# Optimization experiments

Hardware: AMD Instinct MI355X
Metric: run time of the kernel (lower is better)

Reference implementation:

```python
import jax, jax.numpy as jnp
import numpy as np

D_MODEL = 1024
NUM_HEADS = 16
HEAD = D_MODEL // NUM_HEADS
SCALE = float(np.sqrt(D_MODEL))  # note: sqrt(d_model), as in source
LN_EPS = 1e-5


def setup_inputs() -> dict:
    key = jax.random.key(0)
    ks = jax.random.split(key, 12)
    B, Sq, Skv = 2, 2048, 2048
    s = 0.02
    return {
        "x": jax.random.normal(ks[0], (B, Sq, D_MODEL), jnp.float32),
        "enc_output": jax.random.normal(ks[1], (B, Skv, D_MODEL), jnp.float32),
        "Wq": jax.random.normal(ks[2], (D_MODEL, D_MODEL), jnp.float32) * s,
        "bq": jnp.zeros((D_MODEL,), jnp.float32),
        "Wk": jax.random.normal(ks[3], (D_MODEL, D_MODEL), jnp.float32) * s,
        "bk": jnp.zeros((D_MODEL,), jnp.float32),
        "Wv": jax.random.normal(ks[4], (D_MODEL, D_MODEL), jnp.float32) * s,
        "bv": jnp.zeros((D_MODEL,), jnp.float32),
        "Wo": jax.random.normal(ks[5], (D_MODEL, D_MODEL), jnp.float32) * s,
        "bo": jnp.zeros((D_MODEL,), jnp.float32),
        "gamma": jnp.ones((D_MODEL,), jnp.float32),
        "beta": jnp.zeros((D_MODEL,), jnp.float32),
    }


def _split_heads(t):
    B, S, _ = t.shape
    return t.reshape(B, S, NUM_HEADS, HEAD).transpose(0, 2, 1, 3)  # [B,H,S,hd]


def reference(x, enc_output, Wq, bq, Wk, bk, Wv, bv, Wo, bo, gamma, beta):
    q = _split_heads(x @ Wq.T + bq)           # [B,H,Sq,hd]
    k = _split_heads(enc_output @ Wk.T + bk)  # [B,H,Skv,hd]
    v = _split_heads(enc_output @ Wv.T + bv)  # [B,H,Skv,hd]
    scores = jnp.einsum("bhqd,bhkd->bhqk", q, k) / SCALE
    attn_weights = jax.nn.softmax(scores, axis=-1)  # dropout p=0 -> identity
    ctx = jnp.einsum("bhqk,bhkd->bhqd", attn_weights, v)
    B, H, Sq, hd = ctx.shape
    ctx = ctx.transpose(0, 2, 1, 3).reshape(B, Sq, H * hd)
    proj = ctx @ Wo.T + bo
    y = x + proj
    mu = jnp.mean(y, axis=-1, keepdims=True)
    var = jnp.var(y, axis=-1, keepdims=True)
    out = (y - mu) * jax.lax.rsqrt(var + LN_EPS) * gamma + beta
    return out, attn_weights
```

## Files before the change

kernel.cpp:

```cpp
#include <hip/hip_runtime.h>

typedef __attribute__((ext_vector_type(4))) float f32x4;
typedef __attribute__((ext_vector_type(8))) short bf16x8;
typedef __attribute__((ext_vector_type(4))) short s16x4;
typedef __attribute__((ext_vector_type(4))) unsigned u32x4;
typedef unsigned short u16;

#define GLOAD_LDS16(g, l)                                                      \
  __builtin_amdgcn_global_load_lds(                                            \
      (__attribute__((address_space(1))) const void*)(g),                      \
      (__attribute__((address_space(3))) void*)(l), 16, 0, 0)

static __device__ __forceinline__ u16 f2b(float f) {
  unsigned u = __builtin_bit_cast(unsigned, f);
  unsigned r = (u + 0x7fffu + ((u >> 16) & 1u)) >> 16;
  return (u16)r;
}

static __device__ __forceinline__ unsigned pk2(float lo, float hi) {
  unsigned r;
  asm("v_cvt_pk_bf16_f32 %0, %1, %2" : "=v"(r) : "v"(lo), "v"(hi));
  return r;
}

static __device__ __forceinline__ f32x4 mfma16(bf16x8 a, bf16x8 b, f32x4 c) {
  return __builtin_amdgcn_mfma_f32_16x16x32_bf16(a, b, c, 0, 0, 0);
}

static __device__ __forceinline__ int fsw(int row) {
  return (row & 7) ^ ((row & 8) >> 1);
}

__global__ __launch_bounds__(256) void cvt_bf16(const float* __restrict__ in,
                                                u16* __restrict__ out, int n4) {
  int i = blockIdx.x * 256 + threadIdx.x;
  int stride = gridDim.x * 256;
  for (; i < n4; i += stride) {
    float4 v = ((const float4*)in)[i];
    s16x4 o;
    o[0] = (short)f2b(v.x);
    o[1] = (short)f2b(v.y);
    o[2] = (short)f2b(v.z);
    o[3] = (short)f2b(v.w);
    ((s16x4*)out)[i] = o;
  }
}

__global__ __launch_bounds__(256) void cvt_w4(const float* __restrict__ w0,
                                              const float* __restrict__ w1,
                                              const float* __restrict__ w2,
                                              const float* __restrict__ w3,
                                              u16* __restrict__ o0,
                                              u16* __restrict__ o1,
                                              u16* __restrict__ o2,
                                              u16* __restrict__ o3) {
  int y = blockIdx.y;
  const float* in = (y == 0) ? w0 : (y == 1) ? w1 : (y == 2) ? w2 : w3;
  u16* out = (y == 0) ? o0 : (y == 1) ? o1 : (y == 2) ? o2 : o3;
  const int n4 = 262144;
  int i = blockIdx.x * 256 + threadIdx.x;
  int stride = gridDim.x * 256;
  for (; i < n4; i += stride) {
    float4 v = ((const float4*)in)[i];
    s16x4 o;
    o[0] = (short)f2b(v.x);
    o[1] = (short)f2b(v.y);
    o[2] = (short)f2b(v.z);
    o[3] = (short)f2b(v.w);
    ((s16x4*)out)[i] = o;
  }
}

#define QSCALE 0.0450842200278f
__global__ __launch_bounds__(256) void gemm_qkv3(
    const u16* __restrict__ xb, const u16* __restrict__ eb,
    const u16* __restrict__ Wqb, const u16* __restrict__ Wkb,
    const u16* __restrict__ Wvb, const float* __restrict__ bq,
    const float* __restrict__ bk, const float* __restrict__ bv,
    u16* __restrict__ Qd, u16* __restrict__ Kd, u16* __restrict__ Vtd) {
  __shared__ __align__(16) u16 As[128 * 32];
  __shared__ __align__(16) u16 Bs[128 * 32];
  const int K = 1024;
  int z = blockIdx.z;
  const u16* A = (z == 0) ? xb : eb;
  const u16* W = (z == 0) ? Wqb : (z == 1) ? Wkb : Wvb;
  const float* bias = (z == 0) ? bq : (z == 1) ? bk : bv;

  int tid = threadIdx.x;
  int w = tid >> 6, lane = tid & 63;
  int wr = w >> 1, wc = w & 1;
  int r16 = lane & 15, c4 = lane >> 4;
  int m0 = blockIdx.y * 128, n0 = blockIdx.x * 128;
  int srow = tid >> 2;
  int scol = (tid & 3) * 8;

  f32x4 acc[4][4] = {};

  const u16* ga0 = A + (size_t)(m0 + srow) * K + scol;
  const u16* gb0 = W + (size_t)(n0 + srow) * K + scol;
  char* asb = (char*)As + w * 1024;
  char* bsb = (char*)Bs + w * 1024;

  for (int k0 = 0; k0 < K; k0 += 32) {
    GLOAD_LDS16(ga0 + k0, asb);
    GLOAD_LDS16(ga0 + 64 * K + k0, asb + 4096);
    GLOAD_LDS16(gb0 + k0, bsb);
    GLOAD_LDS16(gb0 + 64 * K + k0, bsb + 4096);
    __syncthreads();
    bf16x8 af[4], bfr[4];
#pragma unroll
    for (int i = 0; i < 4; ++i)
      af[i] = *(const bf16x8*)(As + (wr * 64 + i * 16 + r16) * 32 + c4 * 8);
#pragma unroll
    for (int j = 0; j < 4; ++j)
      bfr[j] = *(const bf16x8*)(Bs + (wc * 64 + j * 16 + r16) * 32 + c4 * 8);
#pragma unroll
    for (int i = 0; i < 4; ++i)
#pragma unroll
      for (int j = 0; j < 4; ++j) acc[i][j] = mfma16(af[i], bfr[j], acc[i][j]);
    __syncthreads();
  }

  if (z < 2) {
    float oscale = (z == 0) ? QSCALE : 1.0f;
    u16* dst = (z == 0) ? Qd : Kd;
#pragma unroll
    for (int i = 0; i < 4; ++i) {
      int m = m0 + wr * 64 + i * 16 + c4 * 4;
      int b = m >> 11, s = m & 2047;
#pragma unroll
      for (int j = 0; j < 4; ++j) {
        int n = n0 + wc * 64 + j * 16 + r16;
        int h = n >> 6, d = n & 63;
        float bv = bias[n];
        u16* dp = dst + (((size_t)(b * 16 + h) * 2048 + s) * 64 + d);
#pragma unroll
        for (int r = 0; r < 4; ++r)
          dp[(size_t)r * 64] = f2b((acc[i][j][r] + bv) * oscale);
      }
    }
  } else {
#pragma unroll
    for (int i = 0; i < 4; ++i) {
      int m = m0 + wr * 64 + i * 16 + c4 * 4;
      int b = m >> 11, s = m & 2047;
#pragma unroll
      for (int j = 0; j < 4; ++j) {
        int n = n0 + wc * 64 + j * 16 + r16;
        int h = n >> 6, d = n & 63;
        float bv = bias[n];
        s16x4 o4;
#pragma unroll
        for (int r = 0; r < 4; ++r) o4[r] = (short)f2b(acc[i][j][r] + bv);
        *(s16x4*)(Vtd + ((size_t)((b * 16 + h) * 64 + d)) * 2048 + s) = o4;
      }
    }
  }
}

__global__ __launch_bounds__(256) void gemm_out(const u16* __restrict__ A,
                                                const u16* __restrict__ W,
                                                const float* __restrict__ bias,
                                                const float* __restrict__ X,
                                                float* __restrict__ Y) {
  __shared__ __align__(16) u16 As[128 * 32];
  __shared__ __align__(16) u16 Bs[128 * 32];
  const int K = 1024;
  int tid = threadIdx.x;
  int w = tid >> 6, lane = tid & 63;
  int wr = w >> 1, wc = w & 1;
  int r16 = lane & 15, c4 = lane >> 4;
  int m0 = blockIdx.y * 128, n0 = blockIdx.x * 128;
  int srow = tid >> 2;
  int scol = (tid & 3) * 8;

  f32x4 acc[4][4] = {};

  const u16* ga0 = A + (size_t)(m0 + srow) * K + scol;
  const u16* gb0 = W + (size_t)(n0 + srow) * K + scol;
  char* asb = (char*)As + w * 1024;
  char* bsb = (char*)Bs + w * 1024;

  for (int k0 = 0; k0 < K; k0 += 32) {
    GLOAD_LDS16(ga0 + k0, asb);
    GLOAD_LDS16(ga0 + 64 * K + k0, asb + 4096);
    GLOAD_LDS16(gb0 + k0, bsb);
    GLOAD_LDS16(gb0 + 64 * K + k0, bsb + 4096);
    __syncthreads();
    bf16x8 af[4], bfr[4];
#pragma unroll
    for (int i = 0; i < 4; ++i)
      af[i] = *(const bf16x8*)(As + (wr * 64 + i * 16 + r16) * 32 + c4 * 8);
#pragma unroll
    for (int j = 0; j < 4; ++j)
      bfr[j] = *(const bf16x8*)(Bs + (wc * 64 + j * 16 + r16) * 32 + c4 * 8);
#pragma unroll
    for (int i = 0; i < 4; ++i)
#pragma unroll
      for (int j = 0; j < 4; ++j) acc[i][j] = mfma16(af[i], bfr[j], acc[i][j]);
    __syncthreads();
  }

#pragma unroll
  for (int i = 0; i < 4; ++i) {
    int m = m0 + wr * 64 + i * 16 + c4 * 4;
#pragma unroll
    for (int j = 0; j < 4; ++j) {
      int n = n0 + wc * 64 + j * 16 + r16;
      float bv = bias[n];
#pragma unroll
      for (int r = 0; r < 4; ++r) {
        size_t idx = (size_t)(m + r) * 1024 + n;
        Y[idx] = acc[i][j][r] + bv + X[idx];
      }
    }
  }
}

__global__ __launch_bounds__(256, 2) void attn_k(const u16* __restrict__ Q,
                                                 const u16* __restrict__ Kg,
                                                 const u16* __restrict__ Vt,
                                                 float* __restrict__ attnw,
                                                 u16* __restrict__ ctx) {
  __shared__ __align__(16) u16 Klds[2][64 * 64];
  __shared__ __align__(16) u16 Vlds[2][64 * 64];

  int tid = threadIdx.x;
  int w = tid >> 6, lane = tid & 63;
  int r16 = lane & 15, c4 = lane >> 4;
  int id = blockIdx.x;
  int bh = id & 31, qt = id >> 5;
  int b = bh >> 4, h = bh & 15;
  int q0 = qt * 128 + w * 32;

  const u16* Qp = Q + ((size_t)bh * 2048 + q0) * 64;
  const u16* Kp = Kg + (size_t)bh * 2048 * 64;
  const u16* Vp = Vt + (size_t)bh * 64 * 2048;

  bf16x8 qf[2][2];
#pragma unroll
  for (int hh = 0; hh < 2; ++hh)
#pragma unroll
    for (int ch = 0; ch < 2; ++ch)
      qf[hh][ch] = *(const bf16x8*)(Qp + (size_t)(hh * 16 + r16) * 64 +
                                    ch * 32 + c4 * 8);

  int perm0 = ((r16 >> 2) << 3) + (r16 & 3);
  int srow0 = w * 8 + (lane >> 3);
  int sc = lane & 7;

#define STAGE_K(bufi, kv)                                                      \
  {                                                                            \
    _Pragma("unroll") for (int i = 0; i < 2; ++i) {                            \
      int row = i * 32 + srow0;                                                \
      int ch = sc ^ fsw(row);                                                  \
      GLOAD_LDS16(Kp + (size_t)((kv) + row) * 64 + ch * 8,                     \
                  (u16*)&Klds[bufi][0] + w * 512 + i * 2048);                  \
    }                                                                          \
  }
#define STAGE_V(bufi, kv)                                                      \
  {                                                                            \
    _Pragma("unroll") for (int i = 0; i < 2; ++i) {                            \
      int row = i * 32 + srow0;                                                \
      int ch = sc ^ fsw(row);                                                  \
      GLOAD_LDS16(Vp + (size_t)row * 2048 + (kv) + ch * 8,                     \
                  (u16*)&Vlds[bufi][0] + w * 512 + i * 2048);                  \
    }                                                                          \
  }
#define LDSF(base, row, chunk)                                                 \
  (*(const bf16x8*)((base) + (row) * 64 + (((chunk) ^ fsw(row)) << 3)))
#define WAIT_BAR(n)                                                            \
  {                                                                            \
    asm volatile("s_waitcnt vmcnt(" #n ")" ::: "memory");                      \
    __builtin_amdgcn_s_barrier();                                              \
  }

  float sumA = 0.f, sumB = 0.f;
  STAGE_K(0, 0);
  WAIT_BAR(0);
  int buf = 0;
  for (int kv0 = 0; kv0 < 2048; kv0 += 64) {
    if (kv0 + 64 < 2048) STAGE_K(buf ^ 1, kv0 + 64);
    const u16* Kb = &Klds[buf][0];
#pragma unroll
    for (int s = 0; s < 2; ++s) {
      int ra = s * 32 + perm0;
      bf16x8 k00 = LDSF(Kb, ra, c4);
      bf16x8 k01 = LDSF(Kb, ra, c4 + 4);
      bf16x8 k10 = LDSF(Kb, ra + 4, c4);
      bf16x8 k11 = LDSF(Kb, ra + 4, c4 + 4);
      f32x4 s0A = {}, s1A = {}, s0B = {}, s1B = {};
      __builtin_amdgcn_s_setprio(1);
      s0A = mfma16(k00, qf[0][0], s0A);
      s0A = mfma16(k01, qf[0][1], s0A);
      s1A = mfma16(k10, qf[0][0], s1A);
      s1A = mfma16(k11, qf[0][1], s1A);
      s0B = mfma16(k00, qf[1][0], s0B);
      s0B = mfma16(k01, qf[1][1], s0B);
      s1B = mfma16(k10, qf[1][0], s1B);
      s1B = mfma16(k11, qf[1][1], s1B);
      __builtin_amdgcn_s_setprio(0);
#pragma unroll
      for (int r = 0; r < 4; ++r) {
        sumA += __builtin_amdgcn_exp2f(s0A[r]) + __builtin_amdgcn_exp2f(s1A[r]);
        sumB += __builtin_amdgcn_exp2f(s0B[r]) + __builtin_amdgcn_exp2f(s1B[r]);
      }
    }
    WAIT_BAR(0);
    buf ^= 1;
  }
  sumA += __shfl_xor(sumA, 16, 64);
  sumA += __shfl_xor(sumA, 32, 64);
  sumB += __shfl_xor(sumB, 16, 64);
  sumB += __shfl_xor(sumB, 32, 64);
  float nlsA = -__log2f(sumA);
  float nlsB = -__log2f(sumB);

  f32x4 oA[4] = {}, oB[4] = {};
  float* apA = attnw + ((size_t)bh * 2048 + q0 + r16) * 2048;
  float* apB = apA + (size_t)16 * 2048;
  STAGE_K(0, 0);
  STAGE_V(0, 0);
  WAIT_BAR(0);
  buf = 0;
  for (int kv0 = 0; kv0 < 2048; kv0 += 64) {
    if (kv0 + 64 < 2048) {
      STAGE_K(buf ^ 1, kv0 + 64);
      STAGE_V(buf ^ 1, kv0 + 64);
    }
    const u16* Kb = &Klds[buf][0];
    const u16* Vb = &Vlds[buf][0];
#pragma unroll
    for (int s = 0; s < 2; ++s) {
      int ra = s * 32 + perm0;
      bf16x8 k00 = LDSF(Kb, ra, c4);
      bf16x8 k01 = LDSF(Kb, ra, c4 + 4);
      bf16x8 k10 = LDSF(Kb, ra + 4, c4);
      bf16x8 k11 = LDSF(Kb, ra + 4, c4 + 4);
      f32x4 s0A = {}, s1A = {}, s0B = {}, s1B = {};
      __builtin_amdgcn_s_setprio(1);
      s0A = mfma16(k00, qf[0][0], s0A);
      s0A = mfma16(k01, qf[0][1], s0A);
      s1A = mfma16(k10, qf[0][0], s1A);
      s1A = mfma16(k11, qf[0][1], s1A);
      s0B = mfma16(k00, qf[1][0], s0B);
      s0B = mfma16(k01, qf[1][1], s0B);
      s1B = mfma16(k10, qf[1][0], s1B);
      s1B = mfma16(k11, qf[1][1], s1B);
      __builtin_amdgcn_s_setprio(0);
      f32x4 p0A, p1A, p0B, p1B;
#pragma unroll
      for (int r = 0; r < 4; ++r) {
        p0A[r] = __builtin_amdgcn_exp2f(s0A[r] + nlsA);
        p1A[r] = __builtin_amdgcn_exp2f(s1A[r] + nlsA);
        p0B[r] = __builtin_amdgcn_exp2f(s0B[r] + nlsB);
        p1B[r] = __builtin_amdgcn_exp2f(s1B[r] + nlsB);
      }
      u32x4 pkA, pkB;
      pkA[0] = pk2(p0A[0], p0A[1]);
      pkA[1] = pk2(p0A[2], p0A[3]);
      pkA[2] = pk2(p1A[0], p1A[1]);
      pkA[3] = pk2(p1A[2], p1A[3]);
      pkB[0] = pk2(p0B[0], p0B[1]);
      pkB[1] = pk2(p0B[2], p0B[3]);
      pkB[2] = pk2(p1B[0], p1B[1]);
      pkB[3] = pk2(p1B[2], p1B[3]);
      bf16x8 pfA = __builtin_bit_cast(bf16x8, pkA);
      bf16x8 pfB = __builtin_bit_cast(bf16x8, pkB);
      bf16x8 v0 = LDSF(Vb, 0 * 16 + r16, s * 4 + c4);
      bf16x8 v1 = LDSF(Vb, 1 * 16 + r16, s * 4 + c4);
      bf16x8 v2 = LDSF(Vb, 2 * 16 + r16, s * 4 + c4);
      bf16x8 v3 = LDSF(Vb, 3 * 16 + r16, s * 4 + c4);
      __builtin_amdgcn_s_setprio(1);
      oA[0] = mfma16(pfA, v0, oA[0]);
      oA[1] = mfma16(pfA, v1, oA[1]);
      oA[2] = mfma16(pfA, v2, oA[2]);
      oA[3] = mfma16(pfA, v3, oA[3]);
      oB[0] = mfma16(pfB, v0, oB[0]);
      oB[1] = mfma16(pfB, v1, oB[1]);
      oB[2] = mfma16(pfB, v2, oB[2]);
      oB[3] = mfma16(pfB, v3, oB[3]);
      __builtin_amdgcn_s_setprio(0);
      int kvc = kv0 + s * 32 + c4 * 8;
      *(f32x4*)(apA + kvc) = p0A;
      *(f32x4*)(apA + kvc + 4) = p1A;
      *(f32x4*)(apB + kvc) = p0B;
      *(f32x4*)(apB + kvc + 4) = p1B;
    }
    WAIT_BAR(8);
    buf ^= 1;
  }

#pragma unroll
  for (int dt = 0; dt < 4; ++dt)
#pragma unroll
    for (int r = 0; r < 4; ++r) {
      ctx[((size_t)(b * 2048 + q0 + c4 * 4 + r)) * 1024 + h * 64 + dt * 16 +
          r16] = f2b(oA[dt][r]);
      ctx[((size_t)(b * 2048 + q0 + 16 + c4 * 4 + r)) * 1024 + h * 64 +
          dt * 16 + r16] = f2b(oB[dt][r]);
    }
#undef STAGE_K
#undef STAGE_V
#undef LDSF
#undef WAIT_BAR
}

__global__ __launch_bounds__(256) void ln_k(const float* __restrict__ Y,
                                            const float* __restrict__ gamma,
                                            const float* __restrict__ beta,
                                            float* __restrict__ out) {
  int row = blockIdx.x * 4 + (threadIdx.x >> 6);
  int lane = threadIdx.x & 63;
  const float* yr = Y + (size_t)row * 1024;
  float4 v[4];
  float sum = 0.f, sq = 0.f;
#pragma unroll
  for (int i = 0; i < 4; ++i) {
    v[i] = *(const float4*)(yr + i * 256 + lane * 4);
    sum += v[i].x + v[i].y + v[i].z + v[i].w;
    sq += v[i].x * v[i].x + v[i].y * v[i].y + v[i].z * v[i].z + v[i].w * v[i].w;
  }
#pragma unroll
  for (int m = 1; m < 64; m <<= 1) {
    sum += __shfl_xor(sum, m, 64);
    sq += __shfl_xor(sq, m, 64);
  }
  float mu = sum * (1.f / 1024.f);
  float var = sq * (1.f / 1024.f) - mu * mu;
  float rs = rsqrtf(var + 1e-5f);
  float* orow = out + (size_t)row * 1024;
#pragma unroll
  for (int i = 0; i < 4; ++i) {
    int c = i * 256 + lane * 4;
    float4 g = *(const float4*)(gamma + c);
    float4 be = *(const float4*)(beta + c);
    float4 o;
    o.x = (v[i].x - mu) * rs * g.x + be.x;
    o.y = (v[i].y - mu) * rs * g.y + be.y;
    o.z = (v[i].z - mu) * rs * g.z + be.z;
    o.w = (v[i].w - mu) * rs * g.w + be.w;
    *(float4*)(orow + c) = o;
  }
}

extern "C" void kernel_launch(void* const* d_in, const int* in_sizes, int n_in,
                              void* d_out, int out_size, void* d_ws,
                              size_t ws_size, hipStream_t stream) {
  const float* x = (const float*)d_in[0];
  const float* enc = (const float*)d_in[1];
  const float* Wq = (const float*)d_in[2];
  const float* bq = (const float*)d_in[3];
  const float* Wk = (const float*)d_in[4];
  const float* bk = (const float*)d_in[5];
  const float* Wv = (const float*)d_in[6];
  const float* bv = (const float*)d_in[7];
  const float* Wo = (const float*)d_in[8];
  const float* bo = (const float*)d_in[9];
  const float* gamma = (const float*)d_in[10];
  const float* beta = (const float*)d_in[11];

  float* out = (float*)d_out;
  float* attnw = out + (size_t)4194304;

  char* ws = (char*)d_ws;
  u16* xb = (u16*)(ws + (size_t)0);
  u16* eb = (u16*)(ws + ((size_t)8 << 20));
  u16* Wqb = (u16*)(ws + ((size_t)16 << 20));
  u16* Wkb = (u16*)(ws + ((size_t)18 << 20));
  u16* Wvb = (u16*)(ws + ((size_t)20 << 20));
  u16* Wob = (u16*)(ws + ((size_t)22 << 20));
  u16* Qws = (u16*)(ws + ((size_t)24 << 20));
  u16* Kws = (u16*)(ws + ((size_t)32 << 20));
  u16* Vt = (u16*)(ws + ((size_t)48 << 20));
  u16* ctx = (u16*)(ws + ((size_t)40 << 20));
  float* Yws = (float*)(ws + (size_t)0);

  cvt_bf16<<<dim3(1024), 256, 0, stream>>>(x, xb, 1048576);
  cvt_bf16<<<dim3(1024), 256, 0, stream>>>(enc, eb, 1048576);
  cvt_w4<<<dim3(256, 4), 256, 0, stream>>>(Wq, Wk, Wv, Wo, Wqb, Wkb, Wvb, Wob);

  gemm_qkv3<<<dim3(8, 32, 3), 256, 0, stream>>>(xb, eb, Wqb, Wkb, Wvb, bq, bk,
                                                bv, Qws, Kws, Vt);

  attn_k<<<dim3(512), 256, 0, stream>>>(Qws, Kws, Vt, attnw, ctx);

  gemm_out<<<dim3(8, 32), 256, 0, stream>>>(ctx, Wob, bo, x, Yws);

  ln_k<<<dim3(1024), 256, 0, stream>>>(Yws, gamma, beta, out);
}
```

Measured before the change: 304.5 us.

## Load V fragments directly from global into registers, bypassing LDS staging

The second attention pass no longer stages V tiles through shared memory. Each wave instead loads its V fragments straight from global memory into registers, double-buffered one 32-column half-step ahead, and the vmcnt wait is raised to account for the extra in-flight loads. This removes LDS traffic and the V share of the barrier-synchronised staging, and halves the attention kernel's LDS footprint. In exchange every wave fetches V redundantly from global/L2 (four waves per block), register pressure rises, and the vmcnt accounting becomes more fragile.

```diff
diff --git a/kernel.cpp b/kernel.cpp
--- a/kernel.cpp
+++ b/kernel.cpp
@@ -223,7 +223,6 @@
                                                  float* __restrict__ attnw,
                                                  u16* __restrict__ ctx) {
   __shared__ __align__(16) u16 Klds[2][64 * 64];
-  __shared__ __align__(16) u16 Vlds[2][64 * 64];
 
   int tid = threadIdx.x;
   int w = tid >> 6, lane = tid & 63;
@@ -248,6 +247,7 @@
   int perm0 = ((r16 >> 2) << 3) + (r16 & 3);
   int srow0 = w * 8 + (lane >> 3);
   int sc = lane & 7;
+  const u16* vbase = Vp + (size_t)r16 * 2048 + c4 * 8;
 
 #define STAGE_K(bufi, kv)                                                      \
   {                                                                            \
@@ -258,21 +258,17 @@
                   (u16*)&Klds[bufi][0] + w * 512 + i * 2048);                  \
     }                                                                          \
   }
-#define STAGE_V(bufi, kv)                                                      \
-  {                                                                            \
-    _Pragma("unroll") for (int i = 0; i < 2; ++i) {                            \
-      int row = i * 32 + srow0;                                                \
-      int ch = sc ^ fsw(row);                                                  \
-      GLOAD_LDS16(Vp + (size_t)row * 2048 + (kv) + ch * 8,                     \
-                  (u16*)&Vlds[bufi][0] + w * 512 + i * 2048);                  \
-    }                                                                          \
-  }
 #define LDSF(base, row, chunk)                                                 \
   (*(const bf16x8*)((base) + (row) * 64 + (((chunk) ^ fsw(row)) << 3)))
 #define WAIT_BAR(n)                                                            \
   {                                                                            \
     asm volatile("s_waitcnt vmcnt(" #n ")" ::: "memory");                      \
     __builtin_amdgcn_s_barrier();                                              \
+  }
+#define VLOAD(dst, kvc)                                                        \
+  {                                                                            \
+    _Pragma("unroll") for (int dt = 0; dt < 4; ++dt) (dst)[dt] =               \
+        *(const bf16x8*)(vbase + (size_t)(dt * 16) * 2048 + (kvc));            \
   }
 
   float sumA = 0.f, sumB = 0.f;
@@ -319,17 +315,14 @@
   f32x4 oA[4] = {}, oB[4] = {};
   float* apA = attnw + ((size_t)bh * 2048 + q0 + r16) * 2048;
   float* apB = apA + (size_t)16 * 2048;
+  bf16x8 vg[4], vh[4];
+  VLOAD(vg, 0);
   STAGE_K(0, 0);
-  STAGE_V(0, 0);
   WAIT_BAR(0);
   buf = 0;
   for (int kv0 = 0; kv0 < 2048; kv0 += 64) {
-    if (kv0 + 64 < 2048) {
-      STAGE_K(buf ^ 1, kv0 + 64);
-      STAGE_V(buf ^ 1, kv0 + 64);
-    }
+    if (kv0 + 64 < 2048) STAGE_K(buf ^ 1, kv0 + 64);
     const u16* Kb = &Klds[buf][0];
-    const u16* Vb = &Vlds[buf][0];
 #pragma unroll
     for (int s = 0; s < 2; ++s) {
       int ra = s * 32 + perm0;
@@ -348,6 +341,12 @@
       s1B = mfma16(k10, qf[1][0], s1B);
       s1B = mfma16(k11, qf[1][1], s1B);
       __builtin_amdgcn_s_setprio(0);
+      int kvn = (kv0 + (s + 1) * 32) & 2047;
+      if (s == 0) {
+        VLOAD(vh, kvn);
+      } else {
+        VLOAD(vg, kvn);
+      }
       f32x4 p0A, p1A, p0B, p1B;
 #pragma unroll
       for (int r = 0; r < 4; ++r) {
@@ -367,19 +366,16 @@
       pkB[3] = pk2(p1B[2], p1B[3]);
       bf16x8 pfA = __builtin_bit_cast(bf16x8, pkA);
       bf16x8 pfB = __builtin_bit_cast(bf16x8, pkB);
-      bf16x8 v0 = LDSF(Vb, 0 * 16 + r16, s * 4 + c4);
-      bf16x8 v1 = LDSF(Vb, 1 * 16 + r16, s * 4 + c4);
-      bf16x8 v2 = LDSF(Vb, 2 * 16 + r16, s * 4 + c4);
-      bf16x8 v3 = LDSF(Vb, 3 * 16 + r16, s * 4 + c4);
+      bf16x8* vcur = (s == 0) ? vg : vh;
       __builtin_amdgcn_s_setprio(1);
-      oA[0] = mfma16(pfA, v0, oA[0]);
-      oA[1] = mfma16(pfA, v1, oA[1]);
-      oA[2] = mfma16(pfA, v2, oA[2]);
-      oA[3] = mfma16(pfA, v3, oA[3]);
-      oB[0] = mfma16(pfB, v0, oB[0]);
-      oB[1] = mfma16(pfB, v1, oB[1]);
-      oB[2] = mfma16(pfB, v2, oB[2]);
-      oB[3] = mfma16(pfB, v3, oB[3]);
+      oA[0] = mfma16(pfA, vcur[0], oA[0]);
+      oA[1] = mfma16(pfA, vcur[1], oA[1]);
+      oA[2] = mfma16(pfA, vcur[2], oA[2]);
+      oA[3] = mfma16(pfA, vcur[3], oA[3]);
+      oB[0] = mfma16(pfB, vcur[0], oB[0]);
+      oB[1] = mfma16(pfB, vcur[1], oB[1]);
+      oB[2] = mfma16(pfB, vcur[2], oB[2]);
+      oB[3] = mfma16(pfB, vcur[3], oB[3]);
       __builtin_amdgcn_s_setprio(0);
       int kvc = kv0 + s * 32 + c4 * 8;
       *(f32x4*)(apA + kvc) = p0A;
@@ -387,7 +383,7 @@
       *(f32x4*)(apB + kvc) = p0B;
       *(f32x4*)(apB + kvc + 4) = p1B;
     }
-    WAIT_BAR(8);
+    WAIT_BAR(16);
     buf ^= 1;
   }
 
@@ -401,9 +397,9 @@
           dt * 16 + r16] = f2b(oB[dt][r]);
     }
 #undef STAGE_K
-#undef STAGE_V
 #undef LDSF
 #undef WAIT_BAR
+#undef VLOAD
 }
 
 __global__ __launch_bounds__(256) void ln_k(const float* __restrict__ Y,
```

Result: slower. 345.6 us (+13.5%).

## Split attention KV range across two wave groups with triple-buffered K staging

Applied to the files above, without the earlier changes.

Doubles the attention block to 512 threads. Two groups of four waves each handle half of the 2048-length KV range for the same 128 queries, so the grid keeps the same block count with twice the waves. Partial softmax sums and partial context accumulators are combined through LDS with extra barriers. K staging becomes triple-buffered with deeper prefetch. This raises per-CU parallelism and latency hiding, at the cost of more LDS per block, an LDS reduction step and extra __syncthreads.

```diff
diff --git a/kernel.cpp b/kernel.cpp
--- a/kernel.cpp
+++ b/kernel.cpp
@@ -217,21 +217,23 @@
   }
 }
 
-__global__ __launch_bounds__(256, 2) void attn_k(const u16* __restrict__ Q,
+__global__ __launch_bounds__(512, 4) void attn_k(const u16* __restrict__ Q,
                                                  const u16* __restrict__ Kg,
                                                  const u16* __restrict__ Vt,
                                                  float* __restrict__ attnw,
                                                  u16* __restrict__ ctx) {
-  __shared__ __align__(16) u16 Klds[2][64 * 64];
-  __shared__ __align__(16) u16 Vlds[2][64 * 64];
+  __shared__ __align__(16) u16 Klds[2][3][64 * 64];
+  __shared__ __align__(16) u16 Vlds[2][2][64 * 64];
 
   int tid = threadIdx.x;
   int w = tid >> 6, lane = tid & 63;
+  int g = w >> 2, wq = w & 3;
   int r16 = lane & 15, c4 = lane >> 4;
   int id = blockIdx.x;
   int bh = id & 31, qt = id >> 5;
   int b = bh >> 4, h = bh & 15;
-  int q0 = qt * 128 + w * 32;
+  int q0 = qt * 128 + wq * 32;
+  int kvB = g << 10;
 
   const u16* Qp = Q + ((size_t)bh * 2048 + q0) * 64;
   const u16* Kp = Kg + (size_t)bh * 2048 * 64;
@@ -246,7 +248,7 @@
                                     ch * 32 + c4 * 8);
 
   int perm0 = ((r16 >> 2) << 3) + (r16 & 3);
-  int srow0 = w * 8 + (lane >> 3);
+  int srow0 = wq * 8 + (lane >> 3);
   int sc = lane & 7;
 
 #define STAGE_K(bufi, kv)                                                      \
@@ -254,8 +256,8 @@
     _Pragma("unroll") for (int i = 0; i < 2; ++i) {                            \
       int row = i * 32 + srow0;                                                \
       int ch = sc ^ fsw(row);                                                  \
-      GLOAD_LDS16(Kp + (size_t)((kv) + row) * 64 + ch * 8,                     \
-                  (u16*)&Klds[bufi][0] + w * 512 + i * 2048);                  \
+      GLOAD_LDS16(Kp + (size_t)(kvB + ((kv) & 1023) + row) * 64 + ch * 8,      \
+                  (u16*)&Klds[g][bufi][0] + wq * 512 + i * 2048);              \
     }                                                                          \
   }
 #define STAGE_V(bufi, kv)                                                      \
@@ -263,8 +265,8 @@
     _Pragma("unroll") for (int i = 0; i < 2; ++i) {                            \
       int row = i * 32 + srow0;                                                \
       int ch = sc ^ fsw(row);                                                  \
-      GLOAD_LDS16(Vp + (size_t)row * 2048 + (kv) + ch * 8,                     \
-                  (u16*)&Vlds[bufi][0] + w * 512 + i * 2048);                  \
+      GLOAD_LDS16(Vp + (size_t)row * 2048 + kvB + ((kv) & 1023) + ch * 8,      \
+                  (u16*)&Vlds[g][bufi][0] + wq * 512 + i * 2048);              \
     }                                                                          \
   }
 #define LDSF(base, row, chunk)                                                 \
@@ -277,129 +279,164 @@
 
   float sumA = 0.f, sumB = 0.f;
   STAGE_K(0, 0);
-  WAIT_BAR(0);
-  int buf = 0;
-  for (int kv0 = 0; kv0 < 2048; kv0 += 64) {
-    if (kv0 + 64 < 2048) STAGE_K(buf ^ 1, kv0 + 64);
-    const u16* Kb = &Klds[buf][0];
-#pragma unroll
-    for (int s = 0; s < 2; ++s) {
-      int ra = s * 32 + perm0;
-      bf16x8 k00 = LDSF(Kb, ra, c4);
-      bf16x8 k01 = LDSF(Kb, ra, c4 + 4);
-      bf16x8 k10 = LDSF(Kb, ra + 4, c4);
-      bf16x8 k11 = LDSF(Kb, ra + 4, c4 + 4);
-      f32x4 s0A = {}, s1A = {}, s0B = {}, s1B = {};
-      __builtin_amdgcn_s_setprio(1);
-      s0A = mfma16(k00, qf[0][0], s0A);
-      s0A = mfma16(k01, qf[0][1], s0A);
-      s1A = mfma16(k10, qf[0][0], s1A);
-      s1A = mfma16(k11, qf[0][1], s1A);
-      s0B = mfma16(k00, qf[1][0], s0B);
-      s0B = mfma16(k01, qf[1][1], s0B);
-      s1B = mfma16(k10, qf[1][0], s1B);
-      s1B = mfma16(k11, qf[1][1], s1B);
-      __builtin_amdgcn_s_setprio(0);
-#pragma unroll
-      for (int r = 0; r < 4; ++r) {
-        sumA += __builtin_amdgcn_exp2f(s0A[r]) + __builtin_amdgcn_exp2f(s1A[r]);
-        sumB += __builtin_amdgcn_exp2f(s0B[r]) + __builtin_amdgcn_exp2f(s1B[r]);
+  STAGE_K(1, 64);
+  WAIT_BAR(2);
+  {
+    int wbuf = 2, rbuf = 0;
+    for (int kv0 = 0; kv0 < 1024; kv0 += 64) {
+      STAGE_K(wbuf, kv0 + 128);
+      const u16* Kb = &Klds[g][rbuf][0];
+#pragma unroll
+      for (int s = 0; s < 2; ++s) {
+        int ra = s * 32 + perm0;
+        bf16x8 k00 = LDSF(Kb, ra, c4);
+        bf16x8 k01 = LDSF(Kb, ra, c4 + 4);
+        bf16x8 k10 = LDSF(Kb, ra + 4, c4);
+        bf16x8 k11 = LDSF(Kb, ra + 4, c4 + 4);
+        f32x4 s0A = {}, s1A = {}, s0B = {}, s1B = {};
+        __builtin_amdgcn_s_setprio(1);
+        s0A = mfma16(k00, qf[0][0], s0A);
+        s0A = mfma16(k01, qf[0][1], s0A);
+        s1A = mfma16(k10, qf[0][0], s1A);
+        s1A = mfma16(k11, qf[0][1], s1A);
+        s0B = mfma16(k00, qf[1][0], s0B);
+        s0B = mfma16(k01, qf[1][1], s0B);
+        s1B = mfma16(k10, qf[1][0], s1B);
+        s1B = mfma16(k11, qf[1][1], s1B);
+        __builtin_amdgcn_s_setprio(0);
+#pragma unroll
+        for (int r = 0; r < 4; ++r) {
+          sumA +=
+              __builtin_amdgcn_exp2f(s0A[r]) + __builtin_amdgcn_exp2f(s1A[r]);
+          sumB +=
+              __builtin_amdgcn_exp2f(s0B[r]) + __builtin_amdgcn_exp2f(s1B[r]);
+        }
       }
-    }
-    WAIT_BAR(0);
-    buf ^= 1;
+      WAIT_BAR(2);
+      wbuf = (wbuf == 2) ? 0 : wbuf + 1;
+      rbuf = (rbuf == 2) ? 0 : rbuf + 1;
+    }
   }
   sumA += __shfl_xor(sumA, 16, 64);
   sumA += __shfl_xor(sumA, 32, 64);
   sumB += __shfl_xor(sumB, 16, 64);
   sumB += __shfl_xor(sumB, 32, 64);
-  float nlsA = -__log2f(sumA);
-  float nlsB = -__log2f(sumB);
+
+  float* redbuf = (float*)&Vlds[0][0][0];
+  __syncthreads();
+  if (lane < 16) {
+    redbuf[(g * 4 + wq) * 32 + lane] = sumA;
+    redbuf[(g * 4 + wq) * 32 + 16 + lane] = sumB;
+  }
+  __syncthreads();
+  float nlsA = -__log2f(redbuf[(0 * 4 + wq) * 32 + r16] +
+                        redbuf[(1 * 4 + wq) * 32 + r16]);
+  float nlsB = -__log2f(redbuf[(0 * 4 + wq) * 32 + 16 + r16] +
+                        redbuf[(1 * 4 + wq) * 32 + 16 + r16]);
+  __syncthreads();
 
   f32x4 oA[4] = {}, oB[4] = {};
-  float* apA = attnw + ((size_t)bh * 2048 + q0 + r16) * 2048;
+  float* apA = attnw + ((size_t)bh * 2048 + q0 + r16) * 2048 + kvB;
   float* apB = apA + (size_t)16 * 2048;
+  STAGE_V(0, 0);
   STAGE_K(0, 0);
-  STAGE_V(0, 0);
-  WAIT_BAR(0);
-  buf = 0;
-  for (int kv0 = 0; kv0 < 2048; kv0 += 64) {
-    if (kv0 + 64 < 2048) {
-      STAGE_K(buf ^ 1, kv0 + 64);
-      STAGE_V(buf ^ 1, kv0 + 64);
-    }
-    const u16* Kb = &Klds[buf][0];
-    const u16* Vb = &Vlds[buf][0];
-#pragma unroll
-    for (int s = 0; s < 2; ++s) {
-      int ra = s * 32 + perm0;
-      bf16x8 k00 = LDSF(Kb, ra, c4);
-      bf16x8 k01 = LDSF(Kb, ra, c4 + 4);
-      bf16x8 k10 = LDSF(Kb, ra + 4, c4);
-      bf16x8 k11 = LDSF(Kb, ra + 4, c4 + 4);
-      f32x4 s0A = {}, s1A = {}, s0B = {}, s1B = {};
-      __builtin_amdgcn_s_setprio(1);
-      s0A = mfma16(k00, qf[0][0], s0A);
-      s0A = mfma16(k01, qf[0][1], s0A);
-      s1A = mfma16(k10, qf[0][0], s1A);
-      s1A = mfma16(k11, qf[0][1], s1A);
-      s0B = mfma16(k00, qf[1][0], s0B);
-      s0B = mfma16(k01, qf[1][1], s0B);
-      s1B = mfma16(k10, qf[1][0], s1B);
-      s1B = mfma16(k11, qf[1][1], s1B);
-      __builtin_amdgcn_s_setprio(0);
-      f32x4 p0A, p1A, p0B, p1B;
+  STAGE_K(1, 64);
+  WAIT_BAR(2);
+  {
+    int wbuf = 2, rbuf = 0;
+    int t = 0;
+    for (int kv0 = 0; kv0 < 1024; kv0 += 64, ++t) {
+      STAGE_V((t + 1) & 1, kv0 + 64);
+      STAGE_K(wbuf, kv0 + 128);
+      const u16* Kb = &Klds[g][rbuf][0];
+      const u16* Vb = &Vlds[g][t & 1][0];
+#pragma unroll
+      for (int s = 0; s < 2; ++s) {
+        int ra = s * 32 + perm0;
+        bf16x8 k00 = LDSF(Kb, ra, c4);
+        bf16x8 k01 = LDSF(Kb, ra, c4 + 4);
+        bf16x8 k10 = LDSF(Kb, ra + 4, c4);
+        bf16x8 k11 = LDSF(Kb, ra + 4, c4 + 4);
+        f32x4 s0A = {}, s1A = {}, s0B = {}, s1B = {};
+        __builtin_amdgcn_s_setprio(1);
+        s0A = mfma16(k00, qf[0][0], s0A);
+        s0A = mfma16(k01, qf[0][1], s0A);
+        s1A = mfma16(k10, qf[0][0], s1A);
+        s1A = mfma16(k11, qf[0][1], s1A);
+        s0B = mfma16(k00, qf[1][0], s0B);
+        s0B = mfma16(k01, qf[1][1], s0B);
+        s1B = mfma16(k10, qf[1][0], s1B);
+        s1B = mfma16(k11, qf[1][1], s1B);
+        __builtin_amdgcn_s_setprio(0);
+        f32x4 p0A, p1A, p0B, p1B;
+#pragma unroll
+        for (int r = 0; r < 4; ++r) {
+          p0A[r] = __builtin_amdgcn_exp2f(s0A[r] + nlsA);
+          p1A[r] = __builtin_amdgcn_exp2f(s1A[r] + nlsA);
+          p0B[r] = __builtin_amdgcn_exp2f(s0B[r] + nlsB);
+          p1B[r] = __builtin_amdgcn_exp2f(s1B[r] + nlsB);
+        }
+        u32x4 pkA, pkB;
+        pkA[0] = pk2(p0A[0], p0A[1]);
+        pkA[1] = pk2(p0A[2], p0A[3]);
+        pkA[2] = pk2(p1A[0], p1A[1]);
+        pkA[3] = pk2(p1A[2], p1A[3]);
+        pkB[0] = pk2(p0B[0], p0B[1]);
+        pkB[1] = pk2(p0B[2], p0B[3]);
+        pkB[2] = pk2(p1B[0], p1B[1]);
+        pkB[3] = pk2(p1B[2], p1B[3]);
+        bf16x8 pfA = __builtin_bit_cast(bf16x8, pkA);
+        bf16x8 pfB = __builtin_bit_cast(bf16x8, pkB);
+        bf16x8 v0 = LDSF(Vb, 0 * 16 + r16, s * 4 + c4);
+        bf16x8 v1 = LDSF(Vb, 1 * 16 + r16, s * 4 + c4);
+        bf16x8 v2 = LDSF(Vb, 2 * 16 + r16, s * 4 + c4);
+        bf16x8 v3 = LDSF(Vb, 3 * 16 + r16, s * 4 + c4);
+        __builtin_amdgcn_s_setprio(1);
+        oA[0] = mfma16(pfA, v0, oA[0]);
+        oA[1] = mfma16(pfA, v1, oA[1]);
+        oA[2] = mfma16(pfA, v2, oA[2]);
+        oA[3] = mfma16(pfA, v3, oA[3]);
+        oB[0] = mfma16(pfB, v0, oB[0]);
+        oB[1] = mfma16(pfB, v1, oB[1]);
+        oB[2] = mfma16(pfB, v2, oB[2]);
+        oB[3] = mfma16(pfB, v3, oB[3]);
+        __builtin_amdgcn_s_setprio(0);
+        int kvc = kv0 + s * 32 + c4 * 8;
+        *(f32x4*)(apA + kvc) = p0A;
+        *(f32x4*)(apA + kvc + 4) = p1A;
+        *(f32x4*)(apB + kvc) = p0B;
+        *(f32x4*)(apB + kvc + 4) = p1B;
+      }
+      WAIT_BAR(10);
+      wbuf = (wbuf == 2) ? 0 : wbuf + 1;
+      rbuf = (rbuf == 2) ? 0 : rbuf + 1;
+    }
+  }
+
+  __syncthreads();
+  float* cbuf = (float*)&Klds[0][0][0];
+  if (g == 1) {
+#pragma unroll
+    for (int dt = 0; dt < 4; ++dt) {
+      *(f32x4*)&cbuf[(wq * 64 + lane) * 32 + dt * 4] = oA[dt];
+      *(f32x4*)&cbuf[(wq * 64 + lane) * 32 + 16 + dt * 4] = oB[dt];
+    }
+  }
+  __syncthreads();
+  if (g == 0) {
+#pragma unroll
+    for (int dt = 0; dt < 4; ++dt) {
+      f32x4 o1A = *(const f32x4*)&cbuf[(wq * 64 + lane) * 32 + dt * 4];
+      f32x4 o1B = *(const f32x4*)&cbuf[(wq * 64 + lane) * 32 + 16 + dt * 4];
 #pragma unroll
       for (int r = 0; r < 4; ++r) {
-        p0A[r] = __builtin_amdgcn_exp2f(s0A[r] + nlsA);
-        p1A[r] = __builtin_amdgcn_exp2f(s1A[r] + nlsA);
-        p0B[r] = __builtin_amdgcn_exp2f(s0B[r] + nlsB);
-        p1B[r] = __builtin_amdgcn_exp2f(s1B[r] + nlsB);
+        ctx[((size_t)(b * 2048 + q0 + c4 * 4 + r)) * 1024 + h * 64 + dt * 16 +
+            r16] = f2b(oA[dt][r] + o1A[r]);
+        ctx[((size_t)(b * 2048 + q0 + 16 + c4 * 4 + r)) * 1024 + h * 64 +
+            dt * 16 + r16] = f2b(oB[dt][r] + o1B[r]);
       }
-      u32x4 pkA, pkB;
-      pkA[0] = pk2(p0A[0], p0A[1]);
-      pkA[1] = pk2(p0A[2], p0A[3]);
-      pkA[2] = pk2(p1A[0], p1A[1]);
-      pkA[3] = pk2(p1A[2], p1A[3]);
-      pkB[0] = pk2(p0B[0], p0B[1]);
-      pkB[1] = pk2(p0B[2], p0B[3]);
-      pkB[2] = pk2(p1B[0], p1B[1]);
-      pkB[3] = pk2(p1B[2], p1B[3]);
-      bf16x8 pfA = __builtin_bit_cast(bf16x8, pkA);
-      bf16x8 pfB = __builtin_bit_cast(bf16x8, pkB);
-      bf16x8 v0 = LDSF(Vb, 0 * 16 + r16, s * 4 + c4);
-      bf16x8 v1 = LDSF(Vb, 1 * 16 + r16, s * 4 + c4);
-      bf16x8 v2 = LDSF(Vb, 2 * 16 + r16, s * 4 + c4);
-      bf16x8 v3 = LDSF(Vb, 3 * 16 + r16, s * 4 + c4);
-      __builtin_amdgcn_s_setprio(1);
-      oA[0] = mfma16(pfA, v0, oA[0]);
-      oA[1] = mfma16(pfA, v1, oA[1]);
-      oA[2] = mfma16(pfA, v2, oA[2]);
-      oA[3] = mfma16(pfA, v3, oA[3]);
-      oB[0] = mfma16(pfB, v0, oB[0]);
-      oB[1] = mfma16(pfB, v1, oB[1]);
-      oB[2] = mfma16(pfB, v2, oB[2]);
-      oB[3] = mfma16(pfB, v3, oB[3]);
-      __builtin_amdgcn_s_setprio(0);
-      int kvc = kv0 + s * 32 + c4 * 8;
-      *(f32x4*)(apA + kvc) = p0A;
-      *(f32x4*)(apA + kvc + 4) = p1A;
-      *(f32x4*)(apB + kvc) = p0B;
-      *(f32x4*)(apB + kvc + 4) = p1B;
-    }
-    WAIT_BAR(8);
-    buf ^= 1;
-  }
-
-#pragma unroll
-  for (int dt = 0; dt < 4; ++dt)
-#pragma unroll
-    for (int r = 0; r < 4; ++r) {
-      ctx[((size_t)(b * 2048 + q0 + c4 * 4 + r)) * 1024 + h * 64 + dt * 16 +
-          r16] = f2b(oA[dt][r]);
-      ctx[((size_t)(b * 2048 + q0 + 16 + c4 * 4 + r)) * 1024 + h * 64 +
-          dt * 16 + r16] = f2b(oB[dt][r]);
-    }
+    }
+  }
 #undef STAGE_K
 #undef STAGE_V
 #undef LDSF
@@ -483,7 +520,7 @@
   gemm_qkv3<<<dim3(8, 32, 3), 256, 0, stream>>>(xb, eb, Wqb, Wkb, Wvb, bq, bk,
                                                 bv, Qws, Kws, Vt);
 
-  attn_k<<<dim3(512), 256, 0, stream>>>(Qws, Kws, Vt, attnw, ctx);
+  attn_k<<<dim3(512), 512, 0, stream>>>(Qws, Kws, Vt, attnw, ctx);
 
   gemm_out<<<dim3(8, 32), 256, 0, stream>>>(ctx, Wob, bo, x, Yws);
 
```

After: 277.9 us. -8.8%, faster.
